# Kernel tuning notes

Hardware: AMD Instinct MI355X
Metric: run time of the kernel (lower is better)

Reference implementation:

```python
import jax, jax.numpy as jnp
import numpy as np

N = 50000          # nodes
E = 640000         # edges (before self-loops)
DIM_FEATS = 128
DIM_H = 32
HEADS1 = 8
NUM_CLASS = 16
NEG_SLOPE_ATT = 0.2   # PyG GATv2Conv default negative_slope
NEG_SLOPE_OUT = 0.01  # F.leaky_relu default


def setup_inputs() -> dict:
    key = jax.random.key(0)
    ks = jax.random.split(key, 12)
    s = 0.1
    x = jax.random.normal(ks[0], (N, DIM_FEATS), dtype=jnp.float32)
    edge_index = jax.random.randint(ks[1], (2, E), 0, N, dtype=jnp.int32)
    # GATv2Conv layer 1: dim_feats -> dim_h per head, 8 heads, concat
    W1l = jax.random.normal(ks[2], (DIM_FEATS, HEADS1 * DIM_H), dtype=jnp.float32) * s
    W1r = jax.random.normal(ks[3], (DIM_FEATS, HEADS1 * DIM_H), dtype=jnp.float32) * s
    att1 = jax.random.normal(ks[4], (HEADS1, DIM_H), dtype=jnp.float32) * s
    b1 = jnp.zeros((HEADS1 * DIM_H,), dtype=jnp.float32)
    # GATv2Conv layer 2: 256 -> num_class, 1 head, concat=False
    W2l = jax.random.normal(ks[5], (HEADS1 * DIM_H, NUM_CLASS), dtype=jnp.float32) * s
    W2r = jax.random.normal(ks[6], (HEADS1 * DIM_H, NUM_CLASS), dtype=jnp.float32) * s
    att2 = jax.random.normal(ks[7], (1, NUM_CLASS), dtype=jnp.float32) * s
    b2 = jnp.zeros((NUM_CLASS,), dtype=jnp.float32)
    return {"x": x, "edge_index": edge_index, "W1l": W1l, "W1r": W1r,
            "att1": att1, "b1": b1, "W2l": W2l, "W2r": W2r,
            "att2": att2, "b2": b2}


def _segment_softmax(scores, seg, num_segments):
    # scores: [E, H], seg: [E] destination node ids
    m = jax.ops.segment_max(scores, seg, num_segments=num_segments)  # [N, H]
    e = jnp.exp(scores - m[seg])
    denom = jax.ops.segment_sum(e, seg, num_segments=num_segments)   # [N, H]
    return e / (denom[seg] + 1e-16)


def _gatv2_layer(x, src, dst, Wl, Wr, att, bias, heads, out_ch, concat):
    n = x.shape[0]
    xl = (x @ Wl).reshape(n, heads, out_ch)  # source transform
    xr = (x @ Wr).reshape(n, heads, out_ch)  # target transform
    # per-edge GATv2 score: a^T LeakyReLU(xl[j] + xr[i])
    e = jax.nn.leaky_relu(xl[src] + xr[dst], negative_slope=NEG_SLOPE_ATT)  # [E,H,F]
    alpha = jnp.einsum('ehf,hf->eh', e, att)                                # [E,H]
    alpha = _segment_softmax(alpha, dst, n)
    msg = xl[src] * alpha[:, :, None]                                       # [E,H,F]
    out = jax.ops.segment_sum(msg, dst, num_segments=n)                     # [N,H,F]
    out = out.reshape(n, heads * out_ch) if concat else out.mean(axis=1)
    return out + bias


def reference(x, edge_index, W1l, W1r, att1, b1, W2l, W2r, att2, b2):
    # add_self_loops=True (PyG GATv2Conv default)
    loop = jnp.arange(N, dtype=edge_index.dtype)
    src = jnp.concatenate([edge_index[0], loop])
    dst = jnp.concatenate([edge_index[1], loop])
    # eval mode: all dropouts are identity
    h = _gatv2_layer(x, src, dst, W1l, W1r, att1, b1, HEADS1, DIM_H, concat=True)
    h = jax.nn.elu(h)
    h = _gatv2_layer(h, src, dst, W2l, W2r, att2, b2, 1, NUM_CLASS, concat=False)
    return jax.nn.leaky_relu(h, negative_slope=NEG_SLOPE_OUT)
```

## Files before the change

### kernel.cpp

```cpp
#include <hip/hip_runtime.h>
#include <math.h>

#define NN 50000
#define E0 640000
#define ET 690000
#define F1 128
#define D1 256
#define C2 16
#define NB 196
#define MPAD 50048
#define PADK 136
#define PADK2 264

typedef _Float16 f16x8 __attribute__((ext_vector_type(8)));
typedef _Float16 h2 __attribute__((ext_vector_type(2)));
typedef __attribute__((ext_vector_type(4))) float f32x4;

__device__ __forceinline__ unsigned short f2h(float f) {
  union { _Float16 h; unsigned short u; } c;
  c.h = (_Float16)f;
  return c.u;
}
__device__ __forceinline__ h2 u2h2(unsigned u) {
  union { unsigned u; h2 h; } c; c.u = u; return c.h;
}
__device__ __forceinline__ unsigned h22u(h2 h) {
  union { h2 h; unsigned u; } c; c.h = h; return c.u;
}

__global__ __launch_bounds__(256) void k_cvt_x(const float* __restrict__ x,
                                               unsigned short* __restrict__ xb) {
  long long i = (long long)(blockIdx.x * 256 + threadIdx.x) * 4;
  if (i >= (long long)MPAD * F1) return;
  float4 v = (i < (long long)NN * F1) ? *(const float4*)&x[i]
                                      : make_float4(0.f, 0.f, 0.f, 0.f);
  ushort4 o;
  o.x = f2h(v.x); o.y = f2h(v.y); o.z = f2h(v.z); o.w = f2h(v.w);
  *(ushort4*)&xb[i] = o;
}

__global__ __launch_bounds__(256) void k_cvt_w(
    const float* __restrict__ Wl, const float* __restrict__ Wr,
    const float* __restrict__ W2l, const float* __restrict__ W2r,
    unsigned short* __restrict__ wt, unsigned short* __restrict__ wt2) {
  const int b = blockIdx.x;
  if (b < 256) {
    int tid = b * 256 + threadIdx.x;
    int n = tid >> 7, k = tid & 127;
    float v = (n < 256) ? Wl[k * 256 + n] : Wr[k * 256 + (n - 256)];
    wt[tid] = f2h(v);
  } else {
    int tid = (b - 256) * 256 + threadIdx.x;
    int n = tid >> 8, k = tid & 255;
    float v = (n < 16) ? W2l[k * 16 + n] : W2r[k * 16 + (n - 16)];
    wt2[tid] = f2h(v);
  }
}

__global__ __launch_bounds__(256) void k_gemm1m(
    const unsigned short* __restrict__ xb, const unsigned short* __restrict__ wt,
    unsigned short* __restrict__ xlh, float* __restrict__ xr) {
  __shared__ unsigned short Al[128 * PADK];
  __shared__ unsigned short Bl[128 * PADK];
  const int t = threadIdx.x;
  const int m0 = blockIdx.x * 128;
  const int n0 = blockIdx.y * 128;
  {
    const int r = t >> 4;
    const int c = (t & 15) * 8;
#pragma unroll
    for (int p = 0; p < 8; ++p) {
      const int row = r + p * 16;
      *(float4*)&Al[row * PADK + c] = *(const float4*)&xb[(size_t)(m0 + row) * F1 + c];
      *(float4*)&Bl[row * PADK + c] = *(const float4*)&wt[(size_t)(n0 + row) * F1 + c];
    }
  }
  __syncthreads();
  const int wave = t >> 6, lane = t & 63;
  const int mw = (wave >> 1) * 64, nw = (wave & 1) * 64;
  const int fr = lane & 15, fq = lane >> 4;
  f32x4 acc[4][4] = {};
#pragma unroll
  for (int ks = 0; ks < 4; ++ks) {
    const int ko = ks * 32 + fq * 8;
    f16x8 a[4], b[4];
#pragma unroll
    for (int i = 0; i < 4; ++i)
      a[i] = *(const f16x8*)&Al[(mw + i * 16 + fr) * PADK + ko];
#pragma unroll
    for (int j = 0; j < 4; ++j)
      b[j] = *(const f16x8*)&Bl[(nw + j * 16 + fr) * PADK + ko];
#pragma unroll
    for (int i = 0; i < 4; ++i)
#pragma unroll
      for (int j = 0; j < 4; ++j)
        acc[i][j] = __builtin_amdgcn_mfma_f32_16x16x32_f16(a[i], b[j], acc[i][j], 0, 0, 0);
  }
  if (n0 < 256) {
    const int cb = n0 + nw + fr;
#pragma unroll
    for (int i = 0; i < 4; ++i) {
      const int gm0 = m0 + mw + i * 16 + fq * 4;
#pragma unroll
      for (int j = 0; j < 4; ++j)
#pragma unroll
        for (int r = 0; r < 4; ++r) {
          const int gm = gm0 + r;
          if (gm < NN) xlh[(size_t)gm * D1 + cb + j * 16] = f2h(acc[i][j][r]);
        }
    }
  } else {
    const int cb = (n0 - 256) + nw + fr;
#pragma unroll
    for (int i = 0; i < 4; ++i) {
      const int gm0 = m0 + mw + i * 16 + fq * 4;
#pragma unroll
      for (int j = 0; j < 4; ++j)
#pragma unroll
        for (int r = 0; r < 4; ++r) {
          const int gm = gm0 + r;
          if (gm < NN) xr[(size_t)gm * D1 + cb + j * 16] = acc[i][j][r];
        }
    }
  }
}

__global__ void k_hist(const int* __restrict__ ei, int* __restrict__ deg) {
  int e = blockIdx.x * 256 + threadIdx.x;
  if (e >= ET) return;
  int d = (e < E0) ? ei[E0 + e] : (e - E0);
  atomicAdd(&deg[d], 1);
}

__global__ __launch_bounds__(256) void k_scan_part(const int* __restrict__ deg,
                                                   int* __restrict__ part) {
  int i = blockIdx.x * 256 + threadIdx.x;
  int v = (i < NN) ? deg[i] : 0;
  v += __shfl_xor(v, 1);  v += __shfl_xor(v, 2);  v += __shfl_xor(v, 4);
  v += __shfl_xor(v, 8);  v += __shfl_xor(v, 16); v += __shfl_xor(v, 32);
  __shared__ int w[4];
  if ((threadIdx.x & 63) == 0) w[threadIdx.x >> 6] = v;
  __syncthreads();
  if (threadIdx.x == 0) part[blockIdx.x] = w[0] + w[1] + w[2] + w[3];
}

__global__ __launch_bounds__(256) void k_scan_top(int* __restrict__ part,
                                                  int* __restrict__ offs) {
  __shared__ int lds[256];
  int t = threadIdx.x;
  int v = (t < NB) ? part[t] : 0;
  lds[t] = v;
  __syncthreads();
  for (int off = 1; off < 256; off <<= 1) {
    int u = (t >= off) ? lds[t - off] : 0;
    __syncthreads();
    lds[t] += u;
    __syncthreads();
  }
  if (t < NB) part[t] = lds[t] - v;
  if (t == 255) offs[NN] = lds[255];
}

__global__ __launch_bounds__(256) void k_scan_apply(int* __restrict__ deg,
                                                    const int* __restrict__ part,
                                                    int* __restrict__ offs) {
  __shared__ int lds[256];
  int t = threadIdx.x;
  int i = blockIdx.x * 256 + t;
  int v = (i < NN) ? deg[i] : 0;
  lds[t] = v;
  __syncthreads();
  for (int off = 1; off < 256; off <<= 1) {
    int u = (t >= off) ? lds[t - off] : 0;
    __syncthreads();
    lds[t] += u;
    __syncthreads();
  }
  int excl = lds[t] - v + part[blockIdx.x];
  if (i < NN) { offs[i] = excl; deg[i] = excl; }
}

__global__ void k_scatter(const int* __restrict__ ei, int* __restrict__ cur,
                          int* __restrict__ csr) {
  int e = blockIdx.x * 256 + threadIdx.x;
  if (e >= ET) return;
  int s, d;
  if (e < E0) { s = ei[e]; d = ei[E0 + e]; } else { s = d = e - E0; }
  int pos = atomicAdd(&cur[d], 1);
  csr[pos] = s;
}

__global__ __launch_bounds__(256) void k_agg1(
    const unsigned short* __restrict__ xlh, const float* __restrict__ xr,
    unsigned short* __restrict__ hb,
    const int* __restrict__ offs, const int* __restrict__ csr,
    const float* __restrict__ att, const float* __restrict__ b1) {
  const int wave = threadIdx.x >> 6;
  const int lane = threadIdx.x & 63;
  const int n = blockIdx.x * 4 + wave;
  const int half = lane >> 5;
  const int sub = lane & 31;
  const int col = sub * 8;
  float xr8[8], at8[8];
  *(float4*)&xr8[0] = *(const float4*)&xr[(size_t)n * D1 + col];
  *(float4*)&xr8[4] = *(const float4*)&xr[(size_t)n * D1 + col + 4];
  *(float4*)&at8[0] = *(const float4*)&att[col];
  *(float4*)&at8[4] = *(const float4*)&att[col + 4];
  h2 xrh[4], ath[4];
#pragma unroll
  for (int j = 0; j < 4; ++j) {
    xrh[j] = h2{(_Float16)xr8[2 * j], (_Float16)xr8[2 * j + 1]};
    ath[j] = h2{(_Float16)at8[2 * j], (_Float16)at8[2 * j + 1]};
  }
  float l = 0.f;
  h2 acc2[4] = {h2{0, 0}, h2{0, 0}, h2{0, 0}, h2{0, 0}};
  const int beg = offs[n], fin = offs[n + 1];

  auto body = [&](uint4 w) {
    h2 xh[4];
    xh[0] = u2h2(w.x); xh[1] = u2h2(w.y); xh[2] = u2h2(w.z); xh[3] = u2h2(w.w);
    float c1 = 0.f, c2 = 0.f;
#pragma unroll
    for (int j = 0; j < 4; ++j) {
      h2 v = xh[j] + xrh[j];
      h2 a = u2h2(h22u(v) & 0x7FFF7FFFu);
      c1 = __builtin_amdgcn_fdot2(v, ath[j], c1, false);
      c2 = __builtin_amdgcn_fdot2(a, ath[j], c2, false);
    }
    float c = 0.6f * c1 + 0.4f * c2;
    c += __shfl_xor(c, 1);
    c += __shfl_xor(c, 2);
    const float p = __expf(c);
    l += p;
    const _Float16 ph = (_Float16)p;
    const h2 p2 = h2{ph, ph};
#pragma unroll
    for (int j = 0; j < 4; ++j) acc2[j] += p2 * xh[j];
  };

  int idx = beg + half;
  for (; idx + 2 < fin; idx += 4) {
    const int s0 = csr[idx], s1 = csr[idx + 2];
    const uint4 w0 = *(const uint4*)&xlh[(size_t)s0 * D1 + col];
    const uint4 w1 = *(const uint4*)&xlh[(size_t)s1 * D1 + col];
    body(w0);
    body(w1);
  }
  for (; idx < fin; idx += 2) {
    const int s0 = csr[idx];
    const uint4 w0 = *(const uint4*)&xlh[(size_t)s0 * D1 + col];
    body(w0);
  }
  l += __shfl_xor(l, 32);
#pragma unroll
  for (int j = 0; j < 4; ++j) {
    unsigned u = h22u(acc2[j]);
    u = __shfl_xor((int)u, 32);
    acc2[j] += u2h2(u);
  }
  if (half == 0) {
    const float rl = 1.f / (l + 1e-16f);
    float b8[8], o[8];
    *(float4*)&b8[0] = *(const float4*)&b1[col];
    *(float4*)&b8[4] = *(const float4*)&b1[col + 4];
#pragma unroll
    for (int j = 0; j < 4; ++j) {
      o[2 * j]     = (float)acc2[j][0] * rl + b8[2 * j];
      o[2 * j + 1] = (float)acc2[j][1] * rl + b8[2 * j + 1];
    }
#pragma unroll
    for (int k = 0; k < 8; ++k) o[k] = o[k] > 0.f ? o[k] : expm1f(o[k]);
    ushort4 p0, p1;
    p0.x = f2h(o[0]); p0.y = f2h(o[1]); p0.z = f2h(o[2]); p0.w = f2h(o[3]);
    p1.x = f2h(o[4]); p1.y = f2h(o[5]); p1.z = f2h(o[6]); p1.w = f2h(o[7]);
    *(ushort4*)&hb[(size_t)n * D1 + col] = p0;
    *(ushort4*)&hb[(size_t)n * D1 + col + 4] = p1;
  }
}

__global__ __launch_bounds__(256) void k_gemm2m(
    const unsigned short* __restrict__ hb, const unsigned short* __restrict__ wt2,
    float* __restrict__ h2l, float* __restrict__ h2r) {
  __shared__ unsigned short Bl[32 * PADK2];
  const int t = threadIdx.x;
  {
    const int n = t >> 3, k0 = (t & 7) * 32;
#pragma unroll
    for (int j = 0; j < 4; ++j)
      *(uint4*)&Bl[n * PADK2 + k0 + j * 8] = *(const uint4*)&wt2[n * 256 + k0 + j * 8];
  }
  __syncthreads();
  const int wave = t >> 6, lane = t & 63;
  const int fr = lane & 15, fq = lane >> 4;
  const int m0 = blockIdx.x * 128 + wave * 32;
  f32x4 acc[2][2] = {};
#pragma unroll
  for (int ks = 0; ks < 8; ++ks) {
    const int ko = ks * 32 + fq * 8;
    f16x8 a[2], b[2];
#pragma unroll
    for (int i = 0; i < 2; ++i) {
      int row = m0 + i * 16 + fr; if (row >= NN) row = NN - 1;
      a[i] = *(const f16x8*)&hb[(size_t)row * D1 + ko];
    }
#pragma unroll
    for (int j = 0; j < 2; ++j)
      b[j] = *(const f16x8*)&Bl[(j * 16 + fr) * PADK2 + ko];
#pragma unroll
    for (int i = 0; i < 2; ++i)
#pragma unroll
      for (int j = 0; j < 2; ++j)
        acc[i][j] = __builtin_amdgcn_mfma_f32_16x16x32_f16(a[i], b[j], acc[i][j], 0, 0, 0);
  }
#pragma unroll
  for (int i = 0; i < 2; ++i) {
    const int gm0 = m0 + i * 16 + fq * 4;
#pragma unroll
    for (int r = 0; r < 4; ++r) {
      const int gm = gm0 + r;
      if (gm < NN) {
        h2l[(size_t)gm * C2 + fr] = acc[i][0][r];
        h2r[(size_t)gm * C2 + fr] = acc[i][1][r];
      }
    }
  }
}

__global__ __launch_bounds__(256) void k_agg2(
    const float* __restrict__ h2l, const float* __restrict__ h2r,
    const int* __restrict__ offs, const int* __restrict__ csr,
    const float* __restrict__ att2, const float* __restrict__ b2,
    float* __restrict__ out) {
  const int wave = threadIdx.x >> 6;
  const int lane = threadIdx.x & 63;
  const int n = blockIdx.x * 4 + wave;
  if (n >= NN) return;
  const int c = lane & 15, g = lane >> 4;
  const float xr_v = h2r[(size_t)n * C2 + c];
  const float att_v = att2[c];
  float l = 0.f, acc = 0.f;
  const int beg = offs[n], fin = offs[n + 1];
  for (int idx = beg + g; idx < fin; idx += 4) {
    int s = csr[idx];
    float xlv = h2l[(size_t)s * C2 + c];
    float v = xlv + xr_v;
    v = fmaxf(v, 0.2f * v);
    float sc0 = v * att_v;
    sc0 += __shfl_xor(sc0, 1);
    sc0 += __shfl_xor(sc0, 2);
    sc0 += __shfl_xor(sc0, 4);
    sc0 += __shfl_xor(sc0, 8);
    float p = __expf(sc0);
    l += p;
    acc += p * xlv;
  }
  l += __shfl_xor(l, 16);   l += __shfl_xor(l, 32);
  acc += __shfl_xor(acc, 16); acc += __shfl_xor(acc, 32);
  float o = acc / (l + 1e-16f) + b2[c];
  o = o > 0.f ? o : 0.01f * o;
  if (lane < 16) out[(size_t)n * C2 + c] = o;
}

extern "C" void kernel_launch(void* const* d_in, const int* in_sizes, int n_in,
                              void* d_out, int out_size, void* d_ws, size_t ws_size,
                              hipStream_t stream) {
  const float* x    = (const float*)d_in[0];
  const int*   ei   = (const int*)d_in[1];
  const float* W1l  = (const float*)d_in[2];
  const float* W1r  = (const float*)d_in[3];
  const float* att1 = (const float*)d_in[4];
  const float* b1   = (const float*)d_in[5];
  const float* W2l  = (const float*)d_in[6];
  const float* W2r  = (const float*)d_in[7];
  const float* att2 = (const float*)d_in[8];
  const float* b2   = (const float*)d_in[9];
  float* out = (float*)d_out;

  unsigned short* xlh = (unsigned short*)d_ws;
  float* xr = (float*)(xlh + (size_t)NN * D1);
  unsigned short* hb = (unsigned short*)(xr + (size_t)NN * D1);
  int* deg  = (int*)(hb + (size_t)NN * D1);
  int* offs = deg + NN;
  int* csr  = offs + NN + 1;
  int* part = csr + ET;
  unsigned short* xb = (unsigned short*)(part + NB);
  unsigned short* wt = xb + (size_t)MPAD * F1;
  unsigned short* wt2 = wt + 512 * F1;
  float* h2l = (float*)xlh;
  float* h2r = h2l + (size_t)NN * C2;

  hipMemsetAsync(deg, 0, NN * sizeof(int), stream);
  k_cvt_x<<<(MPAD * F1 / 4 + 255) / 256, 256, 0, stream>>>(x, xb);
  k_cvt_w<<<288, 256, 0, stream>>>(W1l, W1r, W2l, W2r, wt, wt2);
  k_gemm1m<<<dim3(MPAD / 128, 4), 256, 0, stream>>>(xb, wt, xlh, xr);
  k_hist<<<(ET + 255) / 256, 256, 0, stream>>>(ei, deg);
  k_scan_part<<<NB, 256, 0, stream>>>(deg, part);
  k_scan_top<<<1, 256, 0, stream>>>(part, offs);
  k_scan_apply<<<NB, 256, 0, stream>>>(deg, part, offs);
  k_scatter<<<(ET + 255) / 256, 256, 0, stream>>>(ei, deg, csr);
  k_agg1<<<NN / 4, 256, 0, stream>>>(xlh, xr, hb, offs, csr, att1, b1);
  k_gemm2m<<<(NN + 127) / 128, 256, 0, stream>>>(hb, wt2, h2l, h2r);
  k_agg2<<<NN / 4, 256, 0, stream>>>(h2l, h2r, offs, csr, att2, b2, out);
}
```

Baseline: 281.1 us.

## Fuse prep kernels, store xr and layer-2 xl in fp16, fold log2e into attention

```diff
diff --git a/kernel.cpp b/kernel.cpp
--- a/kernel.cpp
+++ b/kernel.cpp
@@ -11,6 +11,7 @@
 #define MPAD 50048
 #define PADK 136
 #define PADK2 264
+#define LOG2E 1.4426950408889634f
 
 typedef _Float16 f16x8 __attribute__((ext_vector_type(8)));
 typedef _Float16 h2 __attribute__((ext_vector_type(2)));
@@ -21,6 +22,9 @@
   c.h = (_Float16)f;
   return c.u;
 }
+__device__ __forceinline__ float h2f(unsigned short u) {
+  union { unsigned short u; _Float16 h; } c; c.u = u; return (float)c.h;
+}
 __device__ __forceinline__ h2 u2h2(unsigned u) {
   union { unsigned u; h2 h; } c; c.u = u; return c.h;
 }
@@ -28,38 +32,42 @@
   union { h2 h; unsigned u; } c; c.h = h; return c.u;
 }
 
-__global__ __launch_bounds__(256) void k_cvt_x(const float* __restrict__ x,
-                                               unsigned short* __restrict__ xb) {
-  long long i = (long long)(blockIdx.x * 256 + threadIdx.x) * 4;
-  if (i >= (long long)MPAD * F1) return;
-  float4 v = (i < (long long)NN * F1) ? *(const float4*)&x[i]
-                                      : make_float4(0.f, 0.f, 0.f, 0.f);
-  ushort4 o;
-  o.x = f2h(v.x); o.y = f2h(v.y); o.z = f2h(v.z); o.w = f2h(v.w);
-  *(ushort4*)&xb[i] = o;
-}
-
-__global__ __launch_bounds__(256) void k_cvt_w(
-    const float* __restrict__ Wl, const float* __restrict__ Wr,
-    const float* __restrict__ W2l, const float* __restrict__ W2r,
-    unsigned short* __restrict__ wt, unsigned short* __restrict__ wt2) {
+__global__ __launch_bounds__(256) void k_prep(
+    const float* __restrict__ x, const float* __restrict__ Wl,
+    const float* __restrict__ Wr, const float* __restrict__ W2l,
+    const float* __restrict__ W2r, const int* __restrict__ ei,
+    unsigned short* __restrict__ xb, unsigned short* __restrict__ wt,
+    unsigned short* __restrict__ wt2, int* __restrict__ deg) {
   const int b = blockIdx.x;
-  if (b < 256) {
-    int tid = b * 256 + threadIdx.x;
+  if (b < 6256) {
+    long long i = (long long)(b * 256 + threadIdx.x) * 4;
+    if (i >= (long long)MPAD * F1) return;
+    float4 v = (i < (long long)NN * F1) ? *(const float4*)&x[i]
+                                        : make_float4(0.f, 0.f, 0.f, 0.f);
+    ushort4 o;
+    o.x = f2h(v.x); o.y = f2h(v.y); o.z = f2h(v.z); o.w = f2h(v.w);
+    *(ushort4*)&xb[i] = o;
+  } else if (b < 6512) {
+    int tid = (b - 6256) * 256 + threadIdx.x;
     int n = tid >> 7, k = tid & 127;
     float v = (n < 256) ? Wl[k * 256 + n] : Wr[k * 256 + (n - 256)];
     wt[tid] = f2h(v);
-  } else {
-    int tid = (b - 256) * 256 + threadIdx.x;
+  } else if (b < 6544) {
+    int tid = (b - 6512) * 256 + threadIdx.x;
     int n = tid >> 8, k = tid & 255;
     float v = (n < 16) ? W2l[k * 16 + n] : W2r[k * 16 + (n - 16)];
     wt2[tid] = f2h(v);
+  } else {
+    int e = (b - 6544) * 256 + threadIdx.x;
+    if (e >= ET) return;
+    int d = (e < E0) ? ei[E0 + e] : (e - E0);
+    atomicAdd(&deg[d], 1);
   }
 }
 
 __global__ __launch_bounds__(256) void k_gemm1m(
     const unsigned short* __restrict__ xb, const unsigned short* __restrict__ wt,
-    unsigned short* __restrict__ xlh, float* __restrict__ xr) {
+    unsigned short* __restrict__ xlh, unsigned short* __restrict__ xrh) {
   __shared__ unsigned short Al[128 * PADK];
   __shared__ unsigned short Bl[128 * PADK];
   const int t = threadIdx.x;
@@ -96,40 +104,19 @@
       for (int j = 0; j < 4; ++j)
         acc[i][j] = __builtin_amdgcn_mfma_f32_16x16x32_f16(a[i], b[j], acc[i][j], 0, 0, 0);
   }
-  if (n0 < 256) {
-    const int cb = n0 + nw + fr;
-#pragma unroll
-    for (int i = 0; i < 4; ++i) {
-      const int gm0 = m0 + mw + i * 16 + fq * 4;
-#pragma unroll
-      for (int j = 0; j < 4; ++j)
-#pragma unroll
-        for (int r = 0; r < 4; ++r) {
-          const int gm = gm0 + r;
-          if (gm < NN) xlh[(size_t)gm * D1 + cb + j * 16] = f2h(acc[i][j][r]);
-        }
-    }
-  } else {
-    const int cb = (n0 - 256) + nw + fr;
-#pragma unroll
-    for (int i = 0; i < 4; ++i) {
-      const int gm0 = m0 + mw + i * 16 + fq * 4;
-#pragma unroll
-      for (int j = 0; j < 4; ++j)
-#pragma unroll
-        for (int r = 0; r < 4; ++r) {
-          const int gm = gm0 + r;
-          if (gm < NN) xr[(size_t)gm * D1 + cb + j * 16] = acc[i][j][r];
-        }
-    }
-  }
-}
-
-__global__ void k_hist(const int* __restrict__ ei, int* __restrict__ deg) {
-  int e = blockIdx.x * 256 + threadIdx.x;
-  if (e >= ET) return;
-  int d = (e < E0) ? ei[E0 + e] : (e - E0);
-  atomicAdd(&deg[d], 1);
+  unsigned short* outp = (n0 < 256) ? xlh : xrh;
+  const int cb = (n0 & 255) + nw + fr;
+#pragma unroll
+  for (int i = 0; i < 4; ++i) {
+    const int gm0 = m0 + mw + i * 16 + fq * 4;
+#pragma unroll
+    for (int j = 0; j < 4; ++j)
+#pragma unroll
+      for (int r = 0; r < 4; ++r) {
+        const int gm = gm0 + r;
+        if (gm < NN) outp[(size_t)gm * D1 + cb + j * 16] = f2h(acc[i][j][r]);
+      }
+  }
 }
 
 __global__ __launch_bounds__(256) void k_scan_part(const int* __restrict__ deg,
@@ -191,7 +178,7 @@
 }
 
 __global__ __launch_bounds__(256) void k_agg1(
-    const unsigned short* __restrict__ xlh, const float* __restrict__ xr,
+    const unsigned short* __restrict__ xlh, const unsigned short* __restrict__ xrh,
     unsigned short* __restrict__ hb,
     const int* __restrict__ offs, const int* __restrict__ csr,
     const float* __restrict__ att, const float* __restrict__ b1) {
@@ -201,16 +188,20 @@
   const int half = lane >> 5;
   const int sub = lane & 31;
   const int col = sub * 8;
-  float xr8[8], at8[8];
-  *(float4*)&xr8[0] = *(const float4*)&xr[(size_t)n * D1 + col];
-  *(float4*)&xr8[4] = *(const float4*)&xr[(size_t)n * D1 + col + 4];
+  const uint4 xru = *(const uint4*)&xrh[(size_t)n * D1 + col];
+  h2 xr2[4];
+  xr2[0] = u2h2(xru.x); xr2[1] = u2h2(xru.y);
+  xr2[2] = u2h2(xru.z); xr2[3] = u2h2(xru.w);
+  float at8[8];
   *(float4*)&at8[0] = *(const float4*)&att[col];
   *(float4*)&at8[4] = *(const float4*)&att[col + 4];
-  h2 xrh[4], ath[4];
+  h2 ath6[4], ath4[4];
 #pragma unroll
   for (int j = 0; j < 4; ++j) {
-    xrh[j] = h2{(_Float16)xr8[2 * j], (_Float16)xr8[2 * j + 1]};
-    ath[j] = h2{(_Float16)at8[2 * j], (_Float16)at8[2 * j + 1]};
+    ath6[j] = h2{(_Float16)(at8[2 * j] * (0.6f * LOG2E)),
+                 (_Float16)(at8[2 * j + 1] * (0.6f * LOG2E))};
+    ath4[j] = h2{(_Float16)(at8[2 * j] * (0.4f * LOG2E)),
+                 (_Float16)(at8[2 * j + 1] * (0.4f * LOG2E))};
   }
   float l = 0.f;
   h2 acc2[4] = {h2{0, 0}, h2{0, 0}, h2{0, 0}, h2{0, 0}};
@@ -219,18 +210,17 @@
   auto body = [&](uint4 w) {
     h2 xh[4];
     xh[0] = u2h2(w.x); xh[1] = u2h2(w.y); xh[2] = u2h2(w.z); xh[3] = u2h2(w.w);
-    float c1 = 0.f, c2 = 0.f;
+    float c = 0.f;
 #pragma unroll
     for (int j = 0; j < 4; ++j) {
-      h2 v = xh[j] + xrh[j];
+      h2 v = xh[j] + xr2[j];
       h2 a = u2h2(h22u(v) & 0x7FFF7FFFu);
-      c1 = __builtin_amdgcn_fdot2(v, ath[j], c1, false);
-      c2 = __builtin_amdgcn_fdot2(a, ath[j], c2, false);
-    }
-    float c = 0.6f * c1 + 0.4f * c2;
+      c = __builtin_amdgcn_fdot2(v, ath6[j], c, false);
+      c = __builtin_amdgcn_fdot2(a, ath4[j], c, false);
+    }
     c += __shfl_xor(c, 1);
     c += __shfl_xor(c, 2);
-    const float p = __expf(c);
+    const float p = exp2f(c);
     l += p;
     const _Float16 ph = (_Float16)p;
     const h2 p2 = h2{ph, ph};
@@ -239,12 +229,14 @@
   };
 
   int idx = beg + half;
-  for (; idx + 2 < fin; idx += 4) {
-    const int s0 = csr[idx], s1 = csr[idx + 2];
+  for (; idx + 4 < fin; idx += 6) {
+    const int s0 = csr[idx], s1 = csr[idx + 2], s2 = csr[idx + 4];
     const uint4 w0 = *(const uint4*)&xlh[(size_t)s0 * D1 + col];
     const uint4 w1 = *(const uint4*)&xlh[(size_t)s1 * D1 + col];
+    const uint4 w2 = *(const uint4*)&xlh[(size_t)s2 * D1 + col];
     body(w0);
     body(w1);
+    body(w2);
   }
   for (; idx < fin; idx += 2) {
     const int s0 = csr[idx];
@@ -280,7 +272,7 @@
 
 __global__ __launch_bounds__(256) void k_gemm2m(
     const unsigned short* __restrict__ hb, const unsigned short* __restrict__ wt2,
-    float* __restrict__ h2l, float* __restrict__ h2r) {
+    unsigned short* __restrict__ h2lh, float* __restrict__ h2r) {
   __shared__ unsigned short Bl[32 * PADK2];
   const int t = threadIdx.x;
   {
@@ -319,7 +311,7 @@
     for (int r = 0; r < 4; ++r) {
       const int gm = gm0 + r;
       if (gm < NN) {
-        h2l[(size_t)gm * C2 + fr] = acc[i][0][r];
+        h2lh[(size_t)gm * C2 + fr] = f2h(acc[i][0][r]);
         h2r[(size_t)gm * C2 + fr] = acc[i][1][r];
       }
     }
@@ -327,7 +319,7 @@
 }
 
 __global__ __launch_bounds__(256) void k_agg2(
-    const float* __restrict__ h2l, const float* __restrict__ h2r,
+    const unsigned short* __restrict__ h2lh, const float* __restrict__ h2r,
     const int* __restrict__ offs, const int* __restrict__ csr,
     const float* __restrict__ att2, const float* __restrict__ b2,
     float* __restrict__ out) {
@@ -337,12 +329,12 @@
   if (n >= NN) return;
   const int c = lane & 15, g = lane >> 4;
   const float xr_v = h2r[(size_t)n * C2 + c];
-  const float att_v = att2[c];
+  const float att_v = att2[c] * LOG2E;
   float l = 0.f, acc = 0.f;
   const int beg = offs[n], fin = offs[n + 1];
   for (int idx = beg + g; idx < fin; idx += 4) {
     int s = csr[idx];
-    float xlv = h2l[(size_t)s * C2 + c];
+    float xlv = h2f(h2lh[(size_t)s * C2 + c]);
     float v = xlv + xr_v;
     v = fmaxf(v, 0.2f * v);
     float sc0 = v * att_v;
@@ -350,9 +342,9 @@
     sc0 += __shfl_xor(sc0, 2);
     sc0 += __shfl_xor(sc0, 4);
     sc0 += __shfl_xor(sc0, 8);
-    float p = __expf(sc0);
+    float p = exp2f(sc0);
     l += p;
-    acc += p * xlv;
+    acc = fmaf(p, xlv, acc);
   }
   l += __shfl_xor(l, 16);   l += __shfl_xor(l, 32);
   acc += __shfl_xor(acc, 16); acc += __shfl_xor(acc, 32);
@@ -377,8 +369,8 @@
   float* out = (float*)d_out;
 
   unsigned short* xlh = (unsigned short*)d_ws;
-  float* xr = (float*)(xlh + (size_t)NN * D1);
-  unsigned short* hb = (unsigned short*)(xr + (size_t)NN * D1);
+  unsigned short* xrh = xlh + (size_t)NN * D1;
+  unsigned short* hb  = xrh + (size_t)NN * D1;
   int* deg  = (int*)(hb + (size_t)NN * D1);
   int* offs = deg + NN;
   int* csr  = offs + NN + 1;
@@ -386,19 +378,18 @@
   unsigned short* xb = (unsigned short*)(part + NB);
   unsigned short* wt = xb + (size_t)MPAD * F1;
   unsigned short* wt2 = wt + 512 * F1;
-  float* h2l = (float*)xlh;
-  float* h2r = h2l + (size_t)NN * C2;
+  unsigned short* h2lh = xlh;
+  float* h2r = (float*)(h2lh + (size_t)NN * C2);
 
   hipMemsetAsync(deg, 0, NN * sizeof(int), stream);
-  k_cvt_x<<<(MPAD * F1 / 4 + 255) / 256, 256, 0, stream>>>(x, xb);
-  k_cvt_w<<<288, 256, 0, stream>>>(W1l, W1r, W2l, W2r, wt, wt2);
-  k_gemm1m<<<dim3(MPAD / 128, 4), 256, 0, stream>>>(xb, wt, xlh, xr);
-  k_hist<<<(ET + 255) / 256, 256, 0, stream>>>(ei, deg);
+  k_prep<<<6544 + (ET + 255) / 256, 256, 0, stream>>>(
+      x, W1l, W1r, W2l, W2r, ei, xb, wt, wt2, deg);
+  k_gemm1m<<<dim3(MPAD / 128, 4), 256, 0, stream>>>(xb, wt, xlh, xrh);
   k_scan_part<<<NB, 256, 0, stream>>>(deg, part);
   k_scan_top<<<1, 256, 0, stream>>>(part, offs);
   k_scan_apply<<<NB, 256, 0, stream>>>(deg, part, offs);
   k_scatter<<<(ET + 255) / 256, 256, 0, stream>>>(ei, deg, csr);
-  k_agg1<<<NN / 4, 256, 0, stream>>>(xlh, xr, hb, offs, csr, att1, b1);
-  k_gemm2m<<<(NN + 127) / 128, 256, 0, stream>>>(hb, wt2, h2l, h2r);
-  k_agg2<<<NN / 4, 256, 0, stream>>>(h2l, h2r, offs, csr, att2, b2, out);
-}
+  k_agg1<<<NN / 4, 256, 0, stream>>>(xlh, xrh, hb, offs, csr, att1, b1);
+  k_gemm2m<<<(NN + 127) / 128, 256, 0, stream>>>(hb, wt2, h2lh, h2r);
+  k_agg2<<<NN / 4, 256, 0, stream>>>(h2lh, h2r, offs, csr, att2, b2, out);
+}
```

Result: faster. 270.5 us (-3.8%).
